# Optimization experiments

Measured on AMD Instinct MI355X. Metric: run time of the kernel, lower is better.

The kernel has to match this reference:

```python
import jax, jax.numpy as jnp
import numpy as np

IGNORE_LABEL = 255
THRESH = 0.7
MIN_KEPT = 262144


def setup_inputs() -> dict:
    key = jax.random.key(0)
    k1, k2 = jax.random.split(key)
    pred = jax.random.normal(k1, (8, 19, 768, 768), dtype=jnp.float32)
    target = jax.random.randint(k2, (8, 768, 768), 0, 19, dtype=jnp.int32)
    return {"pred": pred, "target": target}


def reference(pred, target):
    b, c, h, w = pred.shape
    n = b * h * w

    t = target.reshape(-1)                      # [N]
    valid = t != IGNORE_LABEL                   # [N] bool
    tc = jnp.where(valid, t, 0)                 # clamp ignored labels to 0 for gather
    num_valid = valid.sum()

    # pred.transpose(0,1).reshape(c,-1) in torch flattens (b,h,w) b-major,
    # matching target.view(-1); here we use [N, C] layout instead.
    logits = jnp.transpose(pred, (0, 2, 3, 1)).reshape(n, c)  # [N, C]
    logp = jax.nn.log_softmax(logits, axis=-1)                # [N, C]
    logp_t = jnp.take_along_axis(logp, tc[:, None], axis=-1)[:, 0]  # [N]

    # prob of the ground-truth class; invalid pixels masked to 1 (never "hard")
    mask_prob = jnp.where(valid, jnp.exp(logp_t), 1.0)        # [N]

    # k-th smallest gt-prob defines the OHEM threshold (raised if > thresh)
    k = min(n, MIN_KEPT)
    kth = jnp.sort(mask_prob)[k - 1]
    threshold = jnp.maximum(kth, THRESH)
    kept = mask_prob <= threshold

    # torch: OHEM applies only when min_kept <= num_valid and num_valid > 0
    do_ohem = (num_valid > 0) & (num_valid >= MIN_KEPT)
    valid_f = jnp.where(do_ohem, valid & kept, valid)

    # CrossEntropyLoss(reduction='mean', ignore_index=ignore_label)
    pix_loss = -logp_t                                        # [N]
    denom = jnp.maximum(valid_f.sum(), 1).astype(pred.dtype)
    loss = jnp.sum(jnp.where(valid_f, pix_loss, 0.0)) / denom
    return loss
```

## Files before the change

### kernel.cpp

```cpp
#include <hip/hip_runtime.h>


#define CC 19
#define HWSZ 589824
#define NPIX 4718592
#define KSEL 262144
#define IGNORE_LBL 255
#define THR 0.7f
#define NBLK 1152
#define ITERS 4
#define BIN_07 505

#define W_SPEC_CNT 1
#define W_TOT_CNT 2
#define W_SLOW_CNT 3
#define W_EARLY 4
#define W_SLOW_SUM 6
#define W_SPEC_SUM 8
#define W_TOT_SUM 10
#define HIST1_OFF 16
#define HIST2_OFF (HIST1_OFF + 2048)
#define HIST3_OFF (HIST2_OFF + 2048)
#define META_WORDS 8192
#define PROB_OFF META_WORDS

__global__ __launch_bounds__(256) void k_init(unsigned* __restrict__ ws) {
    for (int i = threadIdx.x; i < META_WORDS; i += 256) ws[i] = 0u;
}

__device__ __forceinline__ bool early_thr(const unsigned* __restrict__ gh) {
    unsigned v = 0;
    for (int i = threadIdx.x; i < BIN_07; i += 256) v += gh[i];
    for (int off = 32; off; off >>= 1) v += __shfl_down(v, off);
    __shared__ unsigned cw[4];
    if ((threadIdx.x & 63) == 0) cw[threadIdx.x >> 6] = v;
    __syncthreads();
    unsigned c_lo = cw[0] + cw[1] + cw[2] + cw[3];
    __syncthreads();
    return c_lo >= (unsigned)KSEL;
}

template <int NBINS>
__device__ __forceinline__ void find_bin(const unsigned* __restrict__ gh,
                                         unsigned krem_in, int shift,
                                         unsigned& sel_io, unsigned& krem_out) {
    constexpr int CHUNK = NBINS / 256;
    __shared__ unsigned csum[256];
    __shared__ unsigned sb[2];
    const int t = threadIdx.x;
    __syncthreads();
    unsigned loc[CHUNK];
    unsigned s = 0;
#pragma unroll
    for (int j = 0; j < CHUNK; ++j) { loc[j] = gh[t * CHUNK + j]; s += loc[j]; }
    csum[t] = s;
    for (int off = 1; off < 256; off <<= 1) {
        __syncthreads();
        unsigned add = (t >= off) ? csum[t - off] : 0u;
        __syncthreads();
        csum[t] += add;
    }
    unsigned incl = csum[t];
    unsigned excl = incl - s;
    if (excl < krem_in && krem_in <= incl) {
        unsigned run = excl;
        unsigned bin = 0;
        bool found = false;
#pragma unroll
        for (int j = 0; j < CHUNK; ++j) {
            unsigned nrun = run + loc[j];
            if (!found && nrun >= krem_in) { bin = (unsigned)(t * CHUNK + j); found = true; }
            if (!found) run = nrun;
        }
        sb[0] = bin;
        sb[1] = krem_in - run;
    }
    __syncthreads();
    sel_io |= sb[0] << shift;
    krem_out = sb[1];
}

__global__ __launch_bounds__(256) void k_pass1(const float* __restrict__ pred,
                                               const int* __restrict__ target,
                                               unsigned* __restrict__ ws) {
    __shared__ unsigned hist[2048];
    for (int i = threadIdx.x; i < 2048; i += 256) hist[i] = 0u;
    __syncthreads();

    float ls_spec = 0.0f, ls_tot = 0.0f;
    unsigned lc_spec = 0, lc_tot = 0;

    for (int it = 0; it < ITERS; ++it) {
        int q = it * (NBLK * 256) + blockIdx.x * 256 + threadIdx.x;
        int pix0 = q * 4;
        int b = pix0 / HWSZ;
        int hw = pix0 - b * HWSZ;
        const float* base = pred + (size_t)b * ((size_t)CC * HWSZ) + hw;

        float x[CC][4];
#pragma unroll
        for (int c = 0; c < CC; ++c) {
            float4 v = *reinterpret_cast<const float4*>(base + (size_t)c * HWSZ);
            x[c][0] = v.x; x[c][1] = v.y; x[c][2] = v.z; x[c][3] = v.w;
        }
        int4 t4 = *reinterpret_cast<const int4*>(target + pix0);
        int tt[4] = {t4.x, t4.y, t4.z, t4.w};

        unsigned pb[4];
#pragma unroll
        for (int p = 0; p < 4; ++p) {
            int t = tt[p];
            bool valid = (t != IGNORE_LBL);
            int tc = valid ? t : 0;
            float m = x[0][p];
#pragma unroll
            for (int c = 1; c < CC; ++c) m = fmaxf(m, x[c][p]);
            float s = 0.0f;
            float xt = x[0][p];
#pragma unroll
            for (int c = 0; c < CC; ++c) {
                float v = x[c][p];
                s += expf(v - m);
                xt = (c == tc) ? v : xt;
            }
            float lp = xt - m - logf(s);
            float pr = valid ? expf(lp) : 1.0f;
            pb[p] = __float_as_uint(pr);
            atomicAdd(&hist[pb[p] >> 21], 1u);
            if (valid) {
                ls_tot += -lp; lc_tot += 1u;
                if (pr <= THR) { ls_spec += -lp; lc_spec += 1u; }
            }
        }
        *reinterpret_cast<uint4*>(ws + PROB_OFF + pix0) =
            make_uint4(pb[0], pb[1], pb[2], pb[3]);
    }

    for (int off = 32; off; off >>= 1) {
        ls_spec += __shfl_down(ls_spec, off);
        ls_tot  += __shfl_down(ls_tot, off);
        lc_spec += __shfl_down(lc_spec, off);
        lc_tot  += __shfl_down(lc_tot, off);
    }
    __shared__ float fs[2][4];
    __shared__ unsigned us[2][4];
    if ((threadIdx.x & 63) == 0) {
        int w = threadIdx.x >> 6;
        fs[0][w] = ls_spec; fs[1][w] = ls_tot;
        us[0][w] = lc_spec; us[1][w] = lc_tot;
    }
    __syncthreads();
    if (threadIdx.x == 0) {
        atomicAdd(reinterpret_cast<double*>(ws + W_SPEC_SUM),
                  (double)(fs[0][0] + fs[0][1] + fs[0][2] + fs[0][3]));
        atomicAdd(reinterpret_cast<double*>(ws + W_TOT_SUM),
                  (double)(fs[1][0] + fs[1][1] + fs[1][2] + fs[1][3]));
        atomicAdd(ws + W_SPEC_CNT, us[0][0] + us[0][1] + us[0][2] + us[0][3]);
        atomicAdd(ws + W_TOT_CNT, us[1][0] + us[1][1] + us[1][2] + us[1][3]);
    }
    int rot = (blockIdx.x & 7) << 8;
    for (int i = threadIdx.x; i < 2048; i += 256) {
        int idx = (i + rot) & 2047;
        unsigned v = hist[idx];
        if (v) atomicAdd(ws + HIST1_OFF + idx, v);
    }
}

template <int LEVEL>
__global__ __launch_bounds__(256) void k_refine(unsigned* __restrict__ ws) {
    if (early_thr(ws + HIST1_OFF)) return;

    constexpr int NB = (LEVEL == 2) ? 2048 : 1024;
    __shared__ unsigned hist[NB];
    for (int i = threadIdx.x; i < NB; i += 256) hist[i] = 0u;
    unsigned sel = 0, krem = 0;
    find_bin<2048>(ws + HIST1_OFF, (unsigned)KSEL, 21, sel, krem);
    if (LEVEL == 3) find_bin<2048>(ws + HIST2_OFF, krem, 10, sel, krem);

    const uint4* pbv = reinterpret_cast<const uint4*>(ws + PROB_OFF);
    for (int it = 0; it < ITERS; ++it) {
        int q = it * (NBLK * 256) + blockIdx.x * 256 + threadIdx.x;
        uint4 v = pbv[q];
        unsigned a[4] = {v.x, v.y, v.z, v.w};
#pragma unroll
        for (int p = 0; p < 4; ++p) {
            unsigned bits = a[p];
            if (LEVEL == 2) {
                if ((bits >> 21) == (sel >> 21))
                    atomicAdd(&hist[(bits >> 10) & 2047u], 1u);
            } else {
                if ((bits >> 10) == (sel >> 10))
                    atomicAdd(&hist[bits & 1023u], 1u);
            }
        }
    }
    __syncthreads();
    unsigned* gh = ws + ((LEVEL == 2) ? HIST2_OFF : HIST3_OFF);
    int rot = (blockIdx.x & 3) << 8;
    for (int i = threadIdx.x; i < NB; i += 256) {
        int idx = (i + rot) & (NB - 1);
        unsigned v = hist[idx];
        if (v) atomicAdd(gh + idx, v);
    }
}

__global__ __launch_bounds__(256) void k_final(unsigned* __restrict__ ws,
                                               const int* __restrict__ target) {
    bool early = early_thr(ws + HIST1_OFF);
    unsigned tot_cnt = ws[W_TOT_CNT];
    bool do_ohem = (tot_cnt > 0u) && (tot_cnt >= (unsigned)KSEL);
    if (blockIdx.x == 0 && threadIdx.x == 0) ws[W_EARLY] = early ? 1u : 0u;
    if (early || !do_ohem) return;

    unsigned sel = 0, krem = 0;
    find_bin<2048>(ws + HIST1_OFF, (unsigned)KSEL, 21, sel, krem);
    find_bin<2048>(ws + HIST2_OFF, krem, 10, sel, krem);
    find_bin<1024>(ws + HIST3_OFF, krem, 0, sel, krem);
    float thr = fmaxf(__uint_as_float(sel), THR);

    const uint4* pbv = reinterpret_cast<const uint4*>(ws + PROB_OFF);
    float ls = 0.0f;
    unsigned lc = 0;
    for (int it = 0; it < ITERS; ++it) {
        int q = it * (NBLK * 256) + blockIdx.x * 256 + threadIdx.x;
        int pix0 = q * 4;
        uint4 v = pbv[q];
        int4 t4 = *reinterpret_cast<const int4*>(target + pix0);
        unsigned a[4] = {v.x, v.y, v.z, v.w};
        int tt[4] = {t4.x, t4.y, t4.z, t4.w};
#pragma unroll
        for (int p = 0; p < 4; ++p) {
            bool valid = (tt[p] != IGNORE_LBL);
            float pr = __uint_as_float(a[p]);
            bool vf = valid && (pr <= thr);
            if (vf) { ls += -logf(fmaxf(pr, 1e-37f)); lc += 1u; }
        }
    }
    for (int off = 32; off; off >>= 1) {
        ls += __shfl_down(ls, off);
        lc += __shfl_down(lc, off);
    }
    __shared__ float wsum[4];
    __shared__ unsigned wcnt[4];
    if ((threadIdx.x & 63) == 0) {
        wsum[threadIdx.x >> 6] = ls;
        wcnt[threadIdx.x >> 6] = lc;
    }
    __syncthreads();
    if (threadIdx.x == 0) {
        atomicAdd(reinterpret_cast<double*>(ws + W_SLOW_SUM),
                  (double)(wsum[0] + wsum[1] + wsum[2] + wsum[3]));
        atomicAdd(ws + W_SLOW_CNT, wcnt[0] + wcnt[1] + wcnt[2] + wcnt[3]);
    }
}

__global__ void k_finalize(const unsigned* __restrict__ ws, float* __restrict__ out) {
    if (threadIdx.x == 0 && blockIdx.x == 0) {
        unsigned tot_cnt = ws[W_TOT_CNT];
        bool do_ohem = (tot_cnt > 0u) && (tot_cnt >= (unsigned)KSEL);
        double s;
        unsigned c;
        if (!do_ohem) {
            s = *reinterpret_cast<const double*>(ws + W_TOT_SUM);  c = tot_cnt;
        } else if (ws[W_EARLY]) {
            s = *reinterpret_cast<const double*>(ws + W_SPEC_SUM); c = ws[W_SPEC_CNT];
        } else {
            s = *reinterpret_cast<const double*>(ws + W_SLOW_SUM); c = ws[W_SLOW_CNT];
        }
        unsigned d = (c > 0u) ? c : 1u;
        out[0] = (float)(s / (double)d);
    }
}

extern "C" void kernel_launch(void* const* d_in, const int* in_sizes, int n_in,
                              void* d_out, int out_size, void* d_ws, size_t ws_size,
                              hipStream_t stream) {
    const float* pred = (const float*)d_in[0];
    const int* target = (const int*)d_in[1];
    unsigned* ws = (unsigned*)d_ws;
    float* out = (float*)d_out;

    k_init<<<1, 256, 0, stream>>>(ws);
    k_pass1<<<NBLK, 256, 0, stream>>>(pred, target, ws);
    k_refine<2><<<NBLK, 256, 0, stream>>>(ws);
    k_refine<3><<<NBLK, 256, 0, stream>>>(ws);
    k_final<<<NBLK, 256, 0, stream>>>(ws, target);
    k_finalize<<<1, 64, 0, stream>>>(ws, out);
}
```

Baseline: 511.7 us.

## Fuse OHEM pipeline into one cooperative persistent kernel with grid syncs

Replaces the chain of six launches (init, pass1, two refine levels, final, finalize) with a single cooperative kernel. It uses grid-stride loops sized from occupancy and cg grid.sync between the histogram-refinement stages. The aim is to remove per-launch overhead and the early-exit launches that do no work. The price is grid-wide barrier costs and a different work distribution (persistent blocks instead of a fixed 1152-block grid). The original multi-kernel path is kept as a fallback if the cooperative launch fails.

```diff
diff --git a/kernel.cpp b/kernel.cpp
--- a/kernel.cpp
+++ b/kernel.cpp
@@ -1,9 +1,13 @@
 #include <hip/hip_runtime.h>
+#include <hip/hip_cooperative_groups.h>
+
+namespace cg = cooperative_groups;
 
 
 #define CC 19
 #define HWSZ 589824
 #define NPIX 4718592
+#define NQUAD (NPIX / 4)
 #define KSEL 262144
 #define IGNORE_LBL 255
 #define THR 0.7f
@@ -24,9 +28,6 @@
 #define META_WORDS 8192
 #define PROB_OFF META_WORDS
 
-__global__ __launch_bounds__(256) void k_init(unsigned* __restrict__ ws) {
-    for (int i = threadIdx.x; i < META_WORDS; i += 256) ws[i] = 0u;
-}
 
 __device__ __forceinline__ bool early_thr(const unsigned* __restrict__ gh) {
     unsigned v = 0;
@@ -80,62 +81,60 @@
     krem_out = sb[1];
 }
 
-__global__ __launch_bounds__(256) void k_pass1(const float* __restrict__ pred,
-                                               const int* __restrict__ target,
-                                               unsigned* __restrict__ ws) {
-    __shared__ unsigned hist[2048];
-    for (int i = threadIdx.x; i < 2048; i += 256) hist[i] = 0u;
-    __syncthreads();
-
-    float ls_spec = 0.0f, ls_tot = 0.0f;
-    unsigned lc_spec = 0, lc_tot = 0;
-
-    for (int it = 0; it < ITERS; ++it) {
-        int q = it * (NBLK * 256) + blockIdx.x * 256 + threadIdx.x;
-        int pix0 = q * 4;
-        int b = pix0 / HWSZ;
-        int hw = pix0 - b * HWSZ;
-        const float* base = pred + (size_t)b * ((size_t)CC * HWSZ) + hw;
-
-        float x[CC][4];
+__device__ __forceinline__ void do_quad(const float* __restrict__ pred,
+                                        const int* __restrict__ target,
+                                        unsigned* __restrict__ ws,
+                                        unsigned* __restrict__ lhist,
+                                        int q, float& ls_spec, float& ls_tot,
+                                        unsigned& lc_spec, unsigned& lc_tot) {
+    int pix0 = q * 4;
+    int b = pix0 / HWSZ;
+    int hw = pix0 - b * HWSZ;
+    const float* base = pred + (size_t)b * ((size_t)CC * HWSZ) + hw;
+
+    float x[CC][4];
+#pragma unroll
+    for (int c = 0; c < CC; ++c) {
+        float4 v = *reinterpret_cast<const float4*>(base + (size_t)c * HWSZ);
+        x[c][0] = v.x; x[c][1] = v.y; x[c][2] = v.z; x[c][3] = v.w;
+    }
+    int4 t4 = *reinterpret_cast<const int4*>(target + pix0);
+    int tt[4] = {t4.x, t4.y, t4.z, t4.w};
+
+    unsigned pb[4];
+#pragma unroll
+    for (int p = 0; p < 4; ++p) {
+        int t = tt[p];
+        bool valid = (t != IGNORE_LBL);
+        int tc = valid ? t : 0;
+        float m = x[0][p];
+#pragma unroll
+        for (int c = 1; c < CC; ++c) m = fmaxf(m, x[c][p]);
+        float s = 0.0f;
+        float xt = x[0][p];
 #pragma unroll
         for (int c = 0; c < CC; ++c) {
-            float4 v = *reinterpret_cast<const float4*>(base + (size_t)c * HWSZ);
-            x[c][0] = v.x; x[c][1] = v.y; x[c][2] = v.z; x[c][3] = v.w;
-        }
-        int4 t4 = *reinterpret_cast<const int4*>(target + pix0);
-        int tt[4] = {t4.x, t4.y, t4.z, t4.w};
-
-        unsigned pb[4];
-#pragma unroll
-        for (int p = 0; p < 4; ++p) {
-            int t = tt[p];
-            bool valid = (t != IGNORE_LBL);
-            int tc = valid ? t : 0;
-            float m = x[0][p];
-#pragma unroll
-            for (int c = 1; c < CC; ++c) m = fmaxf(m, x[c][p]);
-            float s = 0.0f;
-            float xt = x[0][p];
-#pragma unroll
-            for (int c = 0; c < CC; ++c) {
-                float v = x[c][p];
-                s += expf(v - m);
-                xt = (c == tc) ? v : xt;
-            }
-            float lp = xt - m - logf(s);
-            float pr = valid ? expf(lp) : 1.0f;
-            pb[p] = __float_as_uint(pr);
-            atomicAdd(&hist[pb[p] >> 21], 1u);
-            if (valid) {
-                ls_tot += -lp; lc_tot += 1u;
-                if (pr <= THR) { ls_spec += -lp; lc_spec += 1u; }
-            }
-        }
-        *reinterpret_cast<uint4*>(ws + PROB_OFF + pix0) =
-            make_uint4(pb[0], pb[1], pb[2], pb[3]);
-    }
-
+            float v = x[c][p];
+            s += expf(v - m);
+            xt = (c == tc) ? v : xt;
+        }
+        float lp = xt - m - logf(s);
+        float pr = valid ? expf(lp) : 1.0f;
+        pb[p] = __float_as_uint(pr);
+        atomicAdd(&lhist[pb[p] >> 21], 1u);
+        if (valid) {
+            ls_tot += -lp; lc_tot += 1u;
+            if (pr <= THR) { ls_spec += -lp; lc_spec += 1u; }
+        }
+    }
+    *reinterpret_cast<uint4*>(ws + PROB_OFF + pix0) =
+        make_uint4(pb[0], pb[1], pb[2], pb[3]);
+}
+
+__device__ __forceinline__ void flush_pass1(unsigned* __restrict__ ws,
+                                            unsigned* __restrict__ lhist,
+                                            float ls_spec, float ls_tot,
+                                            unsigned lc_spec, unsigned lc_tot) {
     for (int off = 32; off; off >>= 1) {
         ls_spec += __shfl_down(ls_spec, off);
         ls_tot  += __shfl_down(ls_tot, off);
@@ -161,22 +160,159 @@
     int rot = (blockIdx.x & 7) << 8;
     for (int i = threadIdx.x; i < 2048; i += 256) {
         int idx = (i + rot) & 2047;
-        unsigned v = hist[idx];
+        unsigned v = lhist[idx];
         if (v) atomicAdd(ws + HIST1_OFF + idx, v);
     }
+}
+
+
+__global__ __launch_bounds__(256, 4) void k_fused(const float* __restrict__ pred,
+                                                  const int* __restrict__ target,
+                                                  unsigned* __restrict__ ws,
+                                                  float* __restrict__ out) {
+    cg::grid_group grid = cg::this_grid();
+    const int gthreads = (int)gridDim.x * 256;
+    const int gtid = (int)blockIdx.x * 256 + threadIdx.x;
+
+    for (int i = gtid; i < META_WORDS; i += gthreads) ws[i] = 0u;
+
+    __shared__ unsigned hist[2048];
+    for (int i = threadIdx.x; i < 2048; i += 256) hist[i] = 0u;
+    grid.sync();
+
+    float ls_spec = 0.0f, ls_tot = 0.0f;
+    unsigned lc_spec = 0, lc_tot = 0;
+    for (int q = gtid; q < NQUAD; q += gthreads)
+        do_quad(pred, target, ws, hist, q, ls_spec, ls_tot, lc_spec, lc_tot);
+    flush_pass1(ws, hist, ls_spec, ls_tot, lc_spec, lc_tot);
+    grid.sync();
+
+    bool early = early_thr(ws + HIST1_OFF);
+    unsigned tot_cnt = ws[W_TOT_CNT];
+    bool do_ohem = (tot_cnt > 0u) && (tot_cnt >= (unsigned)KSEL);
+    if (early || !do_ohem) {
+        if (blockIdx.x == 0 && threadIdx.x == 0) {
+            double s; unsigned c;
+            if (!do_ohem) { s = *reinterpret_cast<const double*>(ws + W_TOT_SUM);  c = tot_cnt; }
+            else          { s = *reinterpret_cast<const double*>(ws + W_SPEC_SUM); c = ws[W_SPEC_CNT]; }
+            out[0] = (float)(s / (double)((c > 0u) ? c : 1u));
+        }
+        return;
+    }
+
+    const uint4* pbv = reinterpret_cast<const uint4*>(ws + PROB_OFF);
+    unsigned sel = 0, krem = 0;
+
+    for (int i = threadIdx.x; i < 2048; i += 256) hist[i] = 0u;
+    find_bin<2048>(ws + HIST1_OFF, (unsigned)KSEL, 21, sel, krem);
+    for (int q = gtid; q < NQUAD; q += gthreads) {
+        uint4 v = pbv[q];
+        unsigned a[4] = {v.x, v.y, v.z, v.w};
+#pragma unroll
+        for (int p = 0; p < 4; ++p)
+            if ((a[p] >> 21) == (sel >> 21))
+                atomicAdd(&hist[(a[p] >> 10) & 2047u], 1u);
+    }
+    __syncthreads();
+    {
+        int rot = (blockIdx.x & 3) << 8;
+        for (int i = threadIdx.x; i < 2048; i += 256) {
+            int idx = (i + rot) & 2047;
+            unsigned v = hist[idx];
+            if (v) atomicAdd(ws + HIST2_OFF + idx, v);
+        }
+    }
+    grid.sync();
+
+    for (int i = threadIdx.x; i < 1024; i += 256) hist[i] = 0u;
+    find_bin<2048>(ws + HIST2_OFF, krem, 10, sel, krem);
+    for (int q = gtid; q < NQUAD; q += gthreads) {
+        uint4 v = pbv[q];
+        unsigned a[4] = {v.x, v.y, v.z, v.w};
+#pragma unroll
+        for (int p = 0; p < 4; ++p)
+            if ((a[p] >> 10) == (sel >> 10))
+                atomicAdd(&hist[a[p] & 1023u], 1u);
+    }
+    __syncthreads();
+    {
+        int rot = (blockIdx.x & 3) << 8;
+        for (int i = threadIdx.x; i < 1024; i += 256) {
+            int idx = (i + rot) & 1023;
+            unsigned v = hist[idx];
+            if (v) atomicAdd(ws + HIST3_OFF + idx, v);
+        }
+    }
+    grid.sync();
+
+    find_bin<1024>(ws + HIST3_OFF, krem, 0, sel, krem);
+    float thr = fmaxf(__uint_as_float(sel), THR);
+    float ls = 0.0f;
+    unsigned lc = 0;
+    for (int q = gtid; q < NQUAD; q += gthreads) {
+        int pix0 = q * 4;
+        uint4 v = pbv[q];
+        int4 t4 = *reinterpret_cast<const int4*>(target + pix0);
+        unsigned a[4] = {v.x, v.y, v.z, v.w};
+        int tt[4] = {t4.x, t4.y, t4.z, t4.w};
+#pragma unroll
+        for (int p = 0; p < 4; ++p) {
+            bool valid = (tt[p] != IGNORE_LBL);
+            float pr = __uint_as_float(a[p]);
+            if (valid && pr <= thr) { ls += -logf(fmaxf(pr, 1e-37f)); lc += 1u; }
+        }
+    }
+    for (int off = 32; off; off >>= 1) {
+        ls += __shfl_down(ls, off);
+        lc += __shfl_down(lc, off);
+    }
+    __shared__ float wsum[4];
+    __shared__ unsigned wcnt[4];
+    if ((threadIdx.x & 63) == 0) { wsum[threadIdx.x >> 6] = ls; wcnt[threadIdx.x >> 6] = lc; }
+    __syncthreads();
+    if (threadIdx.x == 0) {
+        atomicAdd(reinterpret_cast<double*>(ws + W_SLOW_SUM),
+                  (double)(wsum[0] + wsum[1] + wsum[2] + wsum[3]));
+        atomicAdd(ws + W_SLOW_CNT, wcnt[0] + wcnt[1] + wcnt[2] + wcnt[3]);
+    }
+    grid.sync();
+
+    if (blockIdx.x == 0 && threadIdx.x == 0) {
+        double s = *reinterpret_cast<const double*>(ws + W_SLOW_SUM);
+        unsigned c = ws[W_SLOW_CNT];
+        out[0] = (float)(s / (double)((c > 0u) ? c : 1u));
+    }
+}
+
+
+__global__ __launch_bounds__(256) void k_init(unsigned* __restrict__ ws) {
+    for (int i = threadIdx.x; i < META_WORDS; i += 256) ws[i] = 0u;
+}
+
+__global__ __launch_bounds__(256) void k_pass1(const float* __restrict__ pred,
+                                               const int* __restrict__ target,
+                                               unsigned* __restrict__ ws) {
+    __shared__ unsigned hist[2048];
+    for (int i = threadIdx.x; i < 2048; i += 256) hist[i] = 0u;
+    __syncthreads();
+    float ls_spec = 0.0f, ls_tot = 0.0f;
+    unsigned lc_spec = 0, lc_tot = 0;
+    for (int it = 0; it < ITERS; ++it) {
+        int q = it * (NBLK * 256) + blockIdx.x * 256 + threadIdx.x;
+        do_quad(pred, target, ws, hist, q, ls_spec, ls_tot, lc_spec, lc_tot);
+    }
+    flush_pass1(ws, hist, ls_spec, ls_tot, lc_spec, lc_tot);
 }
 
 template <int LEVEL>
 __global__ __launch_bounds__(256) void k_refine(unsigned* __restrict__ ws) {
     if (early_thr(ws + HIST1_OFF)) return;
-
     constexpr int NB = (LEVEL == 2) ? 2048 : 1024;
     __shared__ unsigned hist[NB];
     for (int i = threadIdx.x; i < NB; i += 256) hist[i] = 0u;
     unsigned sel = 0, krem = 0;
     find_bin<2048>(ws + HIST1_OFF, (unsigned)KSEL, 21, sel, krem);
     if (LEVEL == 3) find_bin<2048>(ws + HIST2_OFF, krem, 10, sel, krem);
-
     const uint4* pbv = reinterpret_cast<const uint4*>(ws + PROB_OFF);
     for (int it = 0; it < ITERS; ++it) {
         int q = it * (NBLK * 256) + blockIdx.x * 256 + threadIdx.x;
@@ -186,11 +322,9 @@
         for (int p = 0; p < 4; ++p) {
             unsigned bits = a[p];
             if (LEVEL == 2) {
-                if ((bits >> 21) == (sel >> 21))
-                    atomicAdd(&hist[(bits >> 10) & 2047u], 1u);
+                if ((bits >> 21) == (sel >> 21)) atomicAdd(&hist[(bits >> 10) & 2047u], 1u);
             } else {
-                if ((bits >> 10) == (sel >> 10))
-                    atomicAdd(&hist[bits & 1023u], 1u);
+                if ((bits >> 10) == (sel >> 10)) atomicAdd(&hist[bits & 1023u], 1u);
             }
         }
     }
@@ -211,13 +345,11 @@
     bool do_ohem = (tot_cnt > 0u) && (tot_cnt >= (unsigned)KSEL);
     if (blockIdx.x == 0 && threadIdx.x == 0) ws[W_EARLY] = early ? 1u : 0u;
     if (early || !do_ohem) return;
-
     unsigned sel = 0, krem = 0;
     find_bin<2048>(ws + HIST1_OFF, (unsigned)KSEL, 21, sel, krem);
     find_bin<2048>(ws + HIST2_OFF, krem, 10, sel, krem);
     find_bin<1024>(ws + HIST3_OFF, krem, 0, sel, krem);
     float thr = fmaxf(__uint_as_float(sel), THR);
-
     const uint4* pbv = reinterpret_cast<const uint4*>(ws + PROB_OFF);
     float ls = 0.0f;
     unsigned lc = 0;
@@ -232,8 +364,7 @@
         for (int p = 0; p < 4; ++p) {
             bool valid = (tt[p] != IGNORE_LBL);
             float pr = __uint_as_float(a[p]);
-            bool vf = valid && (pr <= thr);
-            if (vf) { ls += -logf(fmaxf(pr, 1e-37f)); lc += 1u; }
+            if (valid && pr <= thr) { ls += -logf(fmaxf(pr, 1e-37f)); lc += 1u; }
         }
     }
     for (int off = 32; off; off >>= 1) {
@@ -242,10 +373,7 @@
     }
     __shared__ float wsum[4];
     __shared__ unsigned wcnt[4];
-    if ((threadIdx.x & 63) == 0) {
-        wsum[threadIdx.x >> 6] = ls;
-        wcnt[threadIdx.x >> 6] = lc;
-    }
+    if ((threadIdx.x & 63) == 0) { wsum[threadIdx.x >> 6] = ls; wcnt[threadIdx.x >> 6] = lc; }
     __syncthreads();
     if (threadIdx.x == 0) {
         atomicAdd(reinterpret_cast<double*>(ws + W_SLOW_SUM),
@@ -258,8 +386,7 @@
     if (threadIdx.x == 0 && blockIdx.x == 0) {
         unsigned tot_cnt = ws[W_TOT_CNT];
         bool do_ohem = (tot_cnt > 0u) && (tot_cnt >= (unsigned)KSEL);
-        double s;
-        unsigned c;
+        double s; unsigned c;
         if (!do_ohem) {
             s = *reinterpret_cast<const double*>(ws + W_TOT_SUM);  c = tot_cnt;
         } else if (ws[W_EARLY]) {
@@ -267,8 +394,7 @@
         } else {
             s = *reinterpret_cast<const double*>(ws + W_SLOW_SUM); c = ws[W_SLOW_CNT];
         }
-        unsigned d = (c > 0u) ? c : 1u;
-        out[0] = (float)(s / (double)d);
+        out[0] = (float)(s / (double)((c > 0u) ? c : 1u));
     }
 }
 
@@ -280,6 +406,19 @@
     unsigned* ws = (unsigned*)d_ws;
     float* out = (float*)d_out;
 
+    int occ = 0;
+    hipError_t qe = hipOccupancyMaxActiveBlocksPerMultiprocessor(
+        &occ, reinterpret_cast<const void*>(k_fused), 256, 0);
+    if (qe == hipSuccess && occ >= 1) {
+        int grid = occ * 256;
+        if (grid > 2048) grid = 2048;
+        void* args[] = {(void*)&pred, (void*)&target, (void*)&ws, (void*)&out};
+        hipError_t le = hipLaunchCooperativeKernel(
+            reinterpret_cast<const void*>(k_fused), dim3(grid), dim3(256),
+            args, 0, stream);
+        if (le == hipSuccess) return;
+    }
+
     k_init<<<1, 256, 0, stream>>>(ws);
     k_pass1<<<NBLK, 256, 0, stream>>>(pred, target, ws);
     k_refine<2><<<NBLK, 256, 0, stream>>>(ws);
```

After: 603.0 us. +17.8%, slower.
